# Performance work log

Hardware: AMD Instinct MI355X
Metric: run time of the kernel (lower is better)

The kernel has to match this reference:

```python
import jax, jax.numpy as jnp
import numpy as np

# SS2D (VMamba) dims
B, H, W, C = 2, 48, 48, 96
D_INNER, D_STATE, DT_RANK, K = 192, 32, 6, 4


def _silu(x):
    return x * jax.nn.sigmoid(x)


def setup_inputs() -> dict:
    key = jax.random.key(0)
    ks = jax.random.split(key, 8)
    inputs = jax.random.normal(ks[0], (B, H, W, C), jnp.float32)
    in_proj_w = jax.random.normal(ks[1], (2 * D_INNER, C), jnp.float32) * 0.02
    conv_w = jax.random.normal(ks[2], (D_INNER, 1, 3, 3), jnp.float32) * 0.1
    conv_b = jnp.zeros((D_INNER,), jnp.float32)
    x_proj_w = jax.random.normal(ks[3], (K, DT_RANK + 2 * D_STATE, D_INNER), jnp.float32) * 0.02
    dt_projs_w = jax.random.normal(ks[4], (K, D_INNER, DT_RANK), jnp.float32) * 0.1
    dt_projs_b = jax.random.uniform(ks[5], (K, D_INNER), jnp.float32, -4.0, -2.0)
    # S4D-real init: A_log[n] = log(n+1), tiled over K*d_inner
    A_logs = jnp.log(jnp.tile(jnp.arange(1, D_STATE + 1, dtype=jnp.float32), (K * D_INNER, 1)))
    Ds = jnp.ones((K * D_INNER,), jnp.float32)
    ln_w = jnp.ones((D_INNER,), jnp.float32)
    ln_b = jnp.zeros((D_INNER,), jnp.float32)
    out_proj_w = jax.random.normal(ks[6], (C, D_INNER), jnp.float32) * 0.02
    return dict(inputs=inputs, in_proj_w=in_proj_w, conv_w=conv_w, conv_b=conv_b,
                x_proj_w=x_proj_w, dt_projs_w=dt_projs_w, dt_projs_b=dt_projs_b,
                A_logs=A_logs, Ds=Ds, ln_w=ln_w, ln_b=ln_b, out_proj_w=out_proj_w)


def _selective_scan(us, deltas, A, Bs, Cs, Ds_kd):
    # us, deltas: (B,K,d,L); Bs, Cs: (B,K,N,L); A: (K,d,N); Ds_kd: (K,d)
    u_l = jnp.moveaxis(us, -1, 0)      # (L,B,K,d)
    d_l = jnp.moveaxis(deltas, -1, 0)  # (L,B,K,d)
    B_l = jnp.moveaxis(Bs, -1, 0)      # (L,B,K,N)
    C_l = jnp.moveaxis(Cs, -1, 0)      # (L,B,K,N)
    h0 = jnp.zeros(us.shape[:3] + (A.shape[-1],), us.dtype)  # (B,K,d,N)

    def step(h, inp):
        u, d, b, c = inp
        dA = jnp.exp(d[..., None] * A)                    # (B,K,d,N)
        h = h * dA + (d * u)[..., None] * b[:, :, None, :]
        y = jnp.einsum('bkdn,bkn->bkd', h, c)
        return h, y

    _, ys = jax.lax.scan(step, h0, (u_l, d_l, B_l, C_l))
    ys = jnp.moveaxis(ys, 0, -1)  # (B,K,d,L)
    return ys + Ds_kd[None, :, :, None] * us


def _ss2d(x, in_proj_w, conv_w, conv_b, x_proj_w, dt_projs_w, dt_projs_b,
          A_logs, Ds, ln_w, ln_b, out_proj_w):
    b, h, w, c = x.shape
    L = h * w
    xz = jnp.einsum('bhwc,ec->bhwe', x, in_proj_w)          # (B,H,W,2*d_inner)
    x_, z = jnp.split(xz, 2, axis=-1)
    # depthwise 3x3 conv (NCHW), SAME padding
    x_ = jnp.transpose(x_, (0, 3, 1, 2))                    # (B,d,H,W)
    x_ = jax.lax.conv_general_dilated(x_, conv_w, (1, 1), 'SAME',
                                      feature_group_count=D_INNER,
                                      dimension_numbers=('NCHW', 'OIHW', 'NCHW'))
    x_ = _silu(x_ + conv_b[None, :, None, None])
    # 4-direction scan inputs
    x_hw = x_.reshape(b, D_INNER, L)
    x_wh = jnp.transpose(x_, (0, 1, 3, 2)).reshape(b, D_INNER, L)
    xs = jnp.stack([x_hw, x_wh], axis=1)                    # (B,2,d,L)
    xs = jnp.concatenate([xs, jnp.flip(xs, axis=-1)], axis=1)  # (B,4,d,L)
    x_dbl = jnp.einsum('bkdl,kcd->bkcl', xs, x_proj_w)      # (B,4,dt_rank+2N,L)
    dts = x_dbl[:, :, :DT_RANK]
    Bs = x_dbl[:, :, DT_RANK:DT_RANK + D_STATE]
    Cs = x_dbl[:, :, DT_RANK + D_STATE:]
    dts = jnp.einsum('bkrl,kdr->bkdl', dts, dt_projs_w)
    deltas = jax.nn.softplus(dts + dt_projs_b[None, :, :, None])
    A = -jnp.exp(A_logs).reshape(K, D_INNER, D_STATE)
    Ds_kd = Ds.reshape(K, D_INNER)
    out_y = _selective_scan(xs, deltas, A, Bs, Cs, Ds_kd)   # (B,4,d,L)
    inv_y = jnp.flip(out_y[:, 2:4], axis=-1)                # (B,2,d,L)
    wh_y = jnp.transpose(out_y[:, 1].reshape(b, D_INNER, w, h), (0, 1, 3, 2)).reshape(b, D_INNER, L)
    invwh_y = jnp.transpose(inv_y[:, 1].reshape(b, D_INNER, w, h), (0, 1, 3, 2)).reshape(b, D_INNER, L)
    y = out_y[:, 0] + inv_y[:, 0] + wh_y + invwh_y          # (B,d,L)
    y = jnp.transpose(y, (0, 2, 1)).reshape(b, h, w, D_INNER)
    # LayerNorm over channel dim
    mu = jnp.mean(y, axis=-1, keepdims=True)
    var = jnp.var(y, axis=-1, keepdims=True)
    y = (y - mu) * jax.lax.rsqrt(var + 1e-5) * ln_w + ln_b
    y = y * _silu(z)
    return jnp.einsum('bhwd,cd->bhwc', y, out_proj_w)


def reference(inputs, in_proj_w, conv_w, conv_b, x_proj_w, dt_projs_w, dt_projs_b,
              A_logs, Ds, ln_w, ln_b, out_proj_w):
    attn = _ss2d(inputs, in_proj_w, conv_w, conv_b, x_proj_w, dt_projs_w,
                 dt_projs_b, A_logs, Ds, ln_w, ln_b, out_proj_w)
    return inputs + attn
```

## Files before the change

### kernel.cpp

```cpp
#include <hip/hip_runtime.h>
#include <math.h>

#define B_ 2
#define H_ 48
#define W_ 48
#define C_ 96
#define D_ 192
#define L_ 2304
#define K_ 4
#define NS 32
#define RK 6
#define CD 70

#define NC 16
#define CL (L_/NC)
#define NCH (B_*K_*D_)

#define BDL (B_*D_*L_)
#define OFF_Z      0
#define OFF_XPRE   (OFF_Z    + BDL)
#define OFF_XHW    (OFF_XPRE + BDL)
#define OFF_XWH    (OFF_XHW  + BDL)
#define OFF_DELTA  (OFF_XWH  + BDL)
#define OFF_BS     (OFF_DELTA+ B_*K_*D_*L_)
#define OFF_CS     (OFF_BS   + B_*K_*L_*NS)
#define OFF_YS     (OFF_CS   + B_*K_*L_*NS)
#define OFF_YF     (OFF_YS   + B_*K_*L_*D_)

#define OFF_DU     OFF_YS

#define OFF_H0     OFF_YF

__device__ __forceinline__ float fexp2(float x) {
    float r; asm("v_exp_f32 %0, %1" : "=v"(r) : "v"(x)); return r;
}

__global__ __launch_bounds__(256) void k1_inproj(const float* __restrict__ x,
        const float* __restrict__ w, float* __restrict__ ws) {
    __shared__ __align__(16) float Xs[24*128];
    int blk = blockIdx.x;
    int b = blk / 288;
    int rem = blk % 288;
    int l0 = (rem >> 2) * 32;
    int es = rem & 3;
    int tid = threadIdx.x;
    const float4* xs4 = (const float4*)(x + (size_t)(b*L_ + l0)*C_);
    #pragma unroll
    for (int it = 0; it < 3; ++it) {
        int i4 = it*256 + tid;
        float4 v = xs4[i4];
        int idx4 = i4*4;
        int p = idx4 / 96, c = idx4 % 96;
        *(float4*)&Xs[(c>>2)*128 + p*4] = v;
    }
    __syncthreads();
    int l = tid & 31, eg = tid >> 5;
    int pos = l0 + l;
    float acc[12];
    #pragma unroll
    for (int i = 0; i < 12; ++i) acc[i] = 0.f;
    const float4* wp[12];
    #pragma unroll
    for (int i = 0; i < 12; ++i) {
        int e = es*96 + eg*12 + i;
        wp[i] = (const float4*)(w + (size_t)e*96);
    }
    for (int q = 0; q < 24; ++q) {
        float4 xr = *(const float4*)&Xs[q*128 + l*4];
        #pragma unroll
        for (int i = 0; i < 12; ++i) {
            float4 wv = wp[i][q];
            acc[i] += xr.x*wv.x + xr.y*wv.y + xr.z*wv.z + xr.w*wv.w;
        }
    }
    if (es < 2) {
        float* xpre = ws + OFF_XPRE;
        #pragma unroll
        for (int i = 0; i < 12; ++i) {
            int e = es*96 + eg*12 + i;
            xpre[(size_t)(b*D_ + e)*L_ + pos] = acc[i];
        }
    } else {
        float* zp = ws + OFF_Z + (size_t)(b*L_ + pos)*D_ + (es-2)*96 + eg*12;
        #pragma unroll
        for (int q = 0; q < 3; ++q)
            *(float4*)&zp[q*4] = make_float4(acc[q*4], acc[q*4+1], acc[q*4+2], acc[q*4+3]);
    }
}

__global__ __launch_bounds__(256) void k2_conv(const float* __restrict__ cw,
        const float* __restrict__ cb, float* __restrict__ ws) {
    __shared__ float img[26*48];
    __shared__ float res[24*49];
    int blk = blockIdx.x;
    int bd = blk >> 1;
    int half = blk & 1;
    int d = bd % D_;
    int hh0 = half * 24;
    int tid = threadIdx.x;
    const float* xp = ws + OFF_XPRE + (size_t)bd*L_;
    for (int it = 0; it < 5; ++it) {
        int idx = it*256 + tid;
        if (idx < 26*48) {
            int gr = hh0 - 1 + idx/48;
            img[idx] = (gr >= 0 && gr < H_) ? xp[gr*48 + idx%48] : 0.f;
        }
    }
    float wr[9];
    #pragma unroll
    for (int j = 0; j < 9; ++j) wr[j] = cw[d*9 + j];
    float bias = cb[d];
    __syncthreads();
    float* hw = ws + OFF_XHW + (size_t)bd*L_ + hh0*48;
    for (int it = 0; it < 5; ++it) {
        int idx = it*256 + tid;
        if (idx < 24*48) {
            int r = idx/48, w0 = idx%48;
            float acc = bias;
            #pragma unroll
            for (int kh = 0; kh < 3; ++kh) {
                #pragma unroll
                for (int kw = 0; kw < 3; ++kw) {
                    int iw = w0 + kw - 1;
                    if (iw >= 0 && iw < W_)
                        acc = fmaf(img[(r+kh)*48 + iw], wr[kh*3 + kw], acc);
                }
            }
            float v = acc / (1.f + __expf(-acc));
            hw[idx] = v;
            res[r*49 + w0] = v;
        }
    }
    __syncthreads();
    float* wh = ws + OFF_XWH + (size_t)bd*L_;
    for (int it = 0; it < 5; ++it) {
        int idx = it*256 + tid;
        if (idx < 24*48) {
            int w0 = idx/24, r = idx%24;
            wh[w0*48 + hh0 + r] = res[r*49 + w0];
        }
    }
}

__global__ __launch_bounds__(256) void k3_xproj(const float* __restrict__ xpw,
        const float* __restrict__ dtw, const float* __restrict__ dtb,
        float* __restrict__ ws) {
    __shared__ __align__(16) float Xs[48*64];
    __shared__ float xd[CD*17];
    int blk = blockIdx.x;
    int b = blk / 576;
    int rem = blk % 576;
    int k = rem / 144;
    int l0 = (rem % 144) * 16;
    int tid = threadIdx.x;
    const float* src = ws + ((k & 1) ? OFF_XWH : OFF_XHW);
    bool flip = (k >= 2);
    #pragma unroll
    for (int it = 0; it < 12; ++it) {
        int idx = it*256 + tid;
        int d = idx >> 4, l = idx & 15;
        int pos = flip ? (L_ - 1 - (l0 + l)) : (l0 + l);
        Xs[(d>>2)*64 + l*4 + (d&3)] = src[(size_t)(b*D_ + d)*L_ + pos];
    }
    __syncthreads();
    int l = tid & 15, cg = tid >> 4;
    {
        float acc[5] = {0.f, 0.f, 0.f, 0.f, 0.f};
        const float4* wp[5];
        #pragma unroll
        for (int i = 0; i < 5; ++i) {
            int c = cg + 16*i;
            if (c >= CD) c = 0;
            wp[i] = (const float4*)(xpw + ((size_t)k*CD + c)*D_);
        }
        for (int q = 0; q < 48; ++q) {
            float4 xr = *(const float4*)&Xs[q*64 + l*4];
            #pragma unroll
            for (int i = 0; i < 5; ++i) {
                float4 wv = wp[i][q];
                acc[i] += xr.x*wv.x + xr.y*wv.y + xr.z*wv.z + xr.w*wv.w;
            }
        }
        #pragma unroll
        for (int i = 0; i < 5; ++i) {
            int c = cg + 16*i;
            if (c < CD) xd[c*17 + l] = acc[i];
        }
    }
    __syncthreads();
    {
        float r[6];
        #pragma unroll
        for (int rr = 0; rr < 6; ++rr) r[rr] = xd[rr*17 + l];
        int bk = b*K_ + k;
        float* dout = ws + OFF_DELTA + (size_t)bk*D_*L_;
        int cch = l0 / CL;
        int lc  = l0 - cch*CL + l;
        float* dup = ws + OFF_DU + ((size_t)(bk*NC + cch))*D_*CL;
        int dg = tid >> 4;
        for (int i = 0; i < 12; ++i) {
            int d = dg*12 + i;
            const float* wdt = dtw + ((size_t)k*D_ + d)*6;
            float acc = dtb[k*D_ + d];
            #pragma unroll
            for (int rr = 0; rr < 6; ++rr) acc = fmaf(r[rr], wdt[rr], acc);
            float sp = fmaxf(acc, 0.f) + log1pf(__expf(-fabsf(acc)));
            dout[(size_t)d*L_ + l0 + l] = sp;
            float uv = Xs[(d>>2)*64 + l*4 + (d&3)];
            dup[(size_t)d*CL + lc] = sp * uv;
        }
    }
    {
        float* Bsp = ws + OFF_BS + ((size_t)(b*K_ + k)*L_ + l0)*NS;
        float* Csp = ws + OFF_CS + ((size_t)(b*K_ + k)*L_ + l0)*NS;
        int n = tid & 31, lq = tid >> 5;
        #pragma unroll
        for (int j = 0; j < 2; ++j) {
            int ll = lq + 8*j;
            Bsp[(size_t)ll*NS + n] = xd[(RK + n)*17 + ll];
            Csp[(size_t)ll*NS + n] = xd[(RK + NS + n)*17 + ll];
        }
    }
}

__global__ __launch_bounds__(512) void k4a_local(const float* __restrict__ Alogs,
        float* __restrict__ ws) {
    __shared__ float Pl[2][NC][NS];
    __shared__ float Hl[2][NC][NS];
    int blk = blockIdx.x;
    int bk = blk / 96;
    int p = blk % 96;
    int k = bk & 3;
    int c = threadIdx.x >> 5;
    int n = threadIdx.x & 31;
    int dA = 2*p;
    float aA2 = -__expf(Alogs[((size_t)k*D_ + dA)*NS + n]) * 1.44269504f;
    float aB2 = -__expf(Alogs[((size_t)k*D_ + dA + 1)*NS + n]) * 1.44269504f;
    const float* dpA = ws + OFF_DELTA + (size_t)(bk*D_ + dA)*L_ + c*CL;
    const float* dpB = dpA + L_;
    const float* duA = ws + OFF_DU + ((size_t)(bk*NC + c)*D_ + dA)*CL;
    const float* duB = duA + CL;
    const float* Bsp = ws + OFF_BS + ((size_t)bk*L_ + c*CL)*NS;
    float hA = 0.f, hB = 0.f, PA = 1.f, PB = 1.f;
    #pragma unroll 4
    for (int l = 0; l < CL; ++l) {
        float dlA = dpA[l], dlB = dpB[l];
        float duAv = duA[l], duBv = duB[l];
        float bn = Bsp[l*NS + n];
        float eA = fexp2(dlA * aA2);
        float eB = fexp2(dlB * aB2);
        hA = fmaf(hA, eA, duAv*bn);
        hB = fmaf(hB, eB, duBv*bn);
        PA *= eA;
        PB *= eB;
    }
    Pl[0][c][n] = PA; Pl[1][c][n] = PB;
    Hl[0][c][n] = hA; Hl[1][c][n] = hB;
    __syncthreads();
    if (threadIdx.x < 64) {
        int ch = threadIdx.x >> 5, nn = threadIdx.x & 31;
        float* H0p = ws + OFF_H0 + (size_t)(bk*D_ + dA + ch)*NC*NS + nn;
        float h = 0.f;
        #pragma unroll
        for (int cc = 0; cc < NC; ++cc) {
            H0p[cc*NS] = h;
            h = fmaf(h, Pl[ch][cc][nn], Hl[ch][cc][nn]);
        }
    }
}

__global__ __launch_bounds__(512) void k4c_scan(const float* __restrict__ Alogs,
        float* __restrict__ ws) {
    __shared__ float yld[CL*32];
    int blk = blockIdx.x;
    int dg = blk % 6;
    int c  = (blk / 6) % NC;
    int bk = blk / (6*NC);
    int k = bk & 3;
    int sw = threadIdx.x >> 5;
    int n  = threadIdx.x & 31;
    int dA = dg*32 + sw;
    int dB = dA + 16;
    float aA2 = -__expf(Alogs[((size_t)k*D_ + dA)*NS + n]) * 1.44269504f;
    float aB2 = -__expf(Alogs[((size_t)k*D_ + dB)*NS + n]) * 1.44269504f;
    const float* dpA = ws + OFF_DELTA + (size_t)(bk*D_ + dA)*L_ + c*CL;
    const float* dpB = dpA + 16*L_;
    const float* duA = ws + OFF_DU + ((size_t)(bk*NC + c)*D_ + dA)*CL;
    const float* duB = duA + 16*CL;
    const float* Bsp = ws + OFF_BS + ((size_t)bk*L_ + c*CL)*NS;
    const float* Csp = ws + OFF_CS + ((size_t)bk*L_ + c*CL)*NS;
    float hA = ws[OFF_H0 + (size_t)(bk*D_ + dA)*NC*NS + c*NS + n];
    float hB = ws[OFF_H0 + (size_t)(bk*D_ + dB)*NC*NS + c*NS + n];
    int g = n >> 3;
    int off = ((g & 1) << 1) | (g >> 1);
    for (int lb = 0; lb < CL; lb += 4) {
        float yA[4], yB[4];
        #pragma unroll
        for (int j = 0; j < 4; ++j) {
            int l = lb + j;
            float dlA = dpA[l], dlB = dpB[l];
            float duAv = duA[l], duBv = duB[l];
            float bn = Bsp[l*NS + n];
            float cn = Csp[l*NS + n];
            hA = fmaf(hA, fexp2(dlA*aA2), duAv*bn);
            hB = fmaf(hB, fexp2(dlB*aB2), duBv*bn);
            yA[j] = hA * cn; yB[j] = hB * cn;
        }
        #pragma unroll
        for (int j = 0; j < 4; ++j) {
            yA[j] += __shfl_xor(yA[j], 16);
            yB[j] += __shfl_xor(yB[j], 16);
        }
        float zA0 = (n & 16) ? yA[1] : yA[0];
        float zA1 = (n & 16) ? yA[3] : yA[2];
        float zB0 = (n & 16) ? yB[1] : yB[0];
        float zB1 = (n & 16) ? yB[3] : yB[2];
        zA0 += __shfl_xor(zA0, 8); zA1 += __shfl_xor(zA1, 8);
        zB0 += __shfl_xor(zB0, 8); zB1 += __shfl_xor(zB1, 8);
        float wA = (n & 8) ? zA1 : zA0;
        float wB = (n & 8) ? zB1 : zB0;
        wA += __shfl_xor(wA, 4); wA += __shfl_xor(wA, 2); wA += __shfl_xor(wA, 1);
        wB += __shfl_xor(wB, 4); wB += __shfl_xor(wB, 2); wB += __shfl_xor(wB, 1);
        if ((n & 7) == 0) {
            yld[(lb + off)*32 + sw]      = wA;
            yld[(lb + off)*32 + sw + 16] = wB;
        }
    }
    __syncthreads();
    float* ysp = ws + OFF_YS + (size_t)blk*(CL*32);
    #pragma unroll
    for (int it = 0; it < 9; ++it) {
        int idx = it*512 + threadIdx.x;
        ysp[idx] = yld[idx];
    }
}

__global__ __launch_bounds__(256) void k56_fused(const float* __restrict__ lnw,
        const float* __restrict__ lnb, const float* __restrict__ dsp,
        const float* __restrict__ w, const float* __restrict__ xin,
        float* __restrict__ out, const float* __restrict__ ws) {
    __shared__ __align__(16) float Ys[48*64];
    __shared__ float redS[16][17];
    __shared__ float redQ[16][17];
    __shared__ float muS[16], rsS[16];
    __shared__ float Dsum[D_];
    __shared__ float outT[16*97];
    int blk = blockIdx.x;
    int b = blk / 144;
    int l0 = (blk % 144) * 16;
    int tid = threadIdx.x;
    int hh = l0 / W_;
    int w0b = l0 % W_;
    if (tid < D_) Dsum[tid] = dsp[tid] + dsp[D_+tid] + dsp[2*D_+tid] + dsp[3*D_+tid];
    const float* ysb = ws + OFF_YS;
    int bk0 = b*K_;
    #pragma unroll
    for (int it = 0; it < 3; ++it) {
        int i4 = it*256 + tid;
        int p = i4 / 48, c48 = i4 % 48;
        int pos    = l0 + p;
        int posr   = L_ - 1 - pos;
        int poswh  = (w0b + p)*H_ + hh;
        int poswhr = L_ - 1 - poswh;
        int dsub = c48 >> 3;
        int doff = (c48 & 7) * 4;
        float4 a  = *(const float4*)&ysb[((((size_t)(bk0+0)*NC + pos   /CL)*6 + dsub)*CL + pos   %CL)*32 + doff];
        float4 bb = *(const float4*)&ysb[((((size_t)(bk0+2)*NC + posr  /CL)*6 + dsub)*CL + posr  %CL)*32 + doff];
        float4 cc = *(const float4*)&ysb[((((size_t)(bk0+1)*NC + poswh /CL)*6 + dsub)*CL + poswh %CL)*32 + doff];
        float4 dd = *(const float4*)&ysb[((((size_t)(bk0+3)*NC + poswhr/CL)*6 + dsub)*CL + poswhr%CL)*32 + doff];
        float4 v = make_float4(a.x+bb.x+cc.x+dd.x, a.y+bb.y+cc.y+dd.y,
                               a.z+bb.z+cc.z+dd.z, a.w+bb.w+cc.w+dd.w);
        *(float4*)&Ys[c48*64 + p*4] = v;
    }
    __syncthreads();
    const float* xhw = ws + OFF_XHW;
    #pragma unroll
    for (int it = 0; it < 12; ++it) {
        int idx = it*256 + tid;
        int d = idx >> 4, p = idx & 15;
        float xv = xhw[(size_t)(b*D_ + d)*L_ + l0 + p];
        Ys[(d>>2)*64 + p*4 + (d&3)] += Dsum[d]*xv;
    }
    __syncthreads();
    {
        int p = tid & 15, g = tid >> 4;
        float s = 0.f, q = 0.f;
        #pragma unroll
        for (int j = 0; j < 3; ++j) {
            int qq = g*3 + j;
            #pragma unroll
            for (int sx = 0; sx < 4; ++sx) {
                float v = Ys[qq*64 + p*4 + sx];
                s += v; q += v*v;
            }
        }
        redS[p][g] = s; redQ[p][g] = q;
    }
    __syncthreads();
    if (tid < 16) {
        float s = 0.f, q = 0.f;
        #pragma unroll
        for (int g = 0; g < 16; ++g) { s += redS[tid][g]; q += redQ[tid][g]; }
        float mu  = s * (1.f/192.f);
        float var = q * (1.f/192.f) - mu*mu;
        muS[tid] = mu;
        rsS[tid] = rsqrtf(var + 1e-5f);
    }
    __syncthreads();
    #pragma unroll
    for (int it = 0; it < 3; ++it) {
        int i4 = it*256 + tid;
        int p = i4 / 48, c48 = i4 % 48;
        int pos = l0 + p;
        float4 v  = *(float4*)&Ys[c48*64 + p*4];
        float4 wv = *(const float4*)(lnw + c48*4);
        float4 bv = *(const float4*)(lnb + c48*4);
        float4 zv = *(const float4*)(ws + OFF_Z + (size_t)(b*L_ + pos)*D_ + c48*4);
        float mu = muS[p], rs = rsS[p];
        float o0 = ((v.x-mu)*rs*wv.x + bv.x) * (zv.x / (1.f + __expf(-zv.x)));
        float o1 = ((v.y-mu)*rs*wv.y + bv.y) * (zv.y / (1.f + __expf(-zv.y)));
        float o2 = ((v.z-mu)*rs*wv.z + bv.z) * (zv.z / (1.f + __expf(-zv.z)));
        float o3 = ((v.w-mu)*rs*wv.w + bv.w) * (zv.w / (1.f + __expf(-zv.w)));
        *(float4*)&Ys[c48*64 + p*4] = make_float4(o0, o1, o2, o3);
    }
    __syncthreads();
    int l = tid & 15, cg = tid >> 4;
    float acc[6];
    #pragma unroll
    for (int i = 0; i < 6; ++i) acc[i] = 0.f;
    const float4* wp[6];
    #pragma unroll
    for (int i = 0; i < 6; ++i) {
        int c = cg*6 + i;
        wp[i] = (const float4*)(w + (size_t)c*D_);
    }
    for (int q = 0; q < 48; ++q) {
        float4 xr = *(const float4*)&Ys[q*64 + l*4];
        #pragma unroll
        for (int i = 0; i < 6; ++i) {
            float4 wv = wp[i][q];
            acc[i] += xr.x*wv.x + xr.y*wv.y + xr.z*wv.z + xr.w*wv.w;
        }
    }
    #pragma unroll
    for (int i = 0; i < 6; ++i) outT[l*97 + cg*6 + i] = acc[i];
    __syncthreads();
    #pragma unroll
    for (int it = 0; it < 6; ++it) {
        int idx = it*256 + tid;
        int p = idx / 96, cc = idx % 96;
        size_t o = (size_t)(b*L_ + l0 + p)*C_ + cc;
        out[o] = xin[o] + outT[p*97 + cc];
    }
}

extern "C" void kernel_launch(void* const* d_in, const int* in_sizes, int n_in,
                              void* d_out, int out_size, void* d_ws, size_t ws_size,
                              hipStream_t stream) {
    const float* x        = (const float*)d_in[0];
    const float* in_proj  = (const float*)d_in[1];
    const float* conv_w   = (const float*)d_in[2];
    const float* conv_b   = (const float*)d_in[3];
    const float* x_proj_w = (const float*)d_in[4];
    const float* dt_w     = (const float*)d_in[5];
    const float* dt_b     = (const float*)d_in[6];
    const float* A_logs   = (const float*)d_in[7];
    const float* Ds       = (const float*)d_in[8];
    const float* ln_w     = (const float*)d_in[9];
    const float* ln_b     = (const float*)d_in[10];
    const float* out_w    = (const float*)d_in[11];
    float* out = (float*)d_out;
    float* ws  = (float*)d_ws;

    k1_inproj <<<576,  256, 0, stream>>>(x, in_proj, ws);
    k2_conv   <<<768,  256, 0, stream>>>(conv_w, conv_b, ws);
    k3_xproj  <<<1152, 256, 0, stream>>>(x_proj_w, dt_w, dt_b, ws);
    k4a_local <<<768,  512, 0, stream>>>(A_logs, ws);
    k4c_scan  <<<768,  512, 0, stream>>>(A_logs, ws);
    k56_fused <<<288,  256, 0, stream>>>(ln_w, ln_b, Ds, out_w, x, out, ws);
}
```

Measured before the change: 286.7 us.

## Fuse chunked scan passes into one kernel keeping chunk carries in LDS

The two-pass chunked selective scan (local chunk pass, then a rescan kernel) becomes one kernel per (b,k,d-pair). Chunk carry states stay in shared memory instead of going through global memory, and delta*u is computed on the fly from the conv output rather than precomputed and stored by the x-projection kernel. Scan outputs are written in a plain (bk,d,L) layout, which simplifies the gather in the final fused kernel. In exchange, each block now runs the delta/B/C reads twice and holds a per-block LDS buffer of L float2 values. The fused scan also has only two channels of parallelism per block instead of the previous 32-channel grouping, which could reduce the available occupancy.

```diff
diff --git a/kernel.cpp b/kernel.cpp
--- a/kernel.cpp
+++ b/kernel.cpp
@@ -14,7 +14,6 @@
 
 #define NC 16
 #define CL (L_/NC)
-#define NCH (B_*K_*D_)
 
 #define BDL (B_*D_*L_)
 #define OFF_Z      0
@@ -25,11 +24,6 @@
 #define OFF_BS     (OFF_DELTA+ B_*K_*D_*L_)
 #define OFF_CS     (OFF_BS   + B_*K_*L_*NS)
 #define OFF_YS     (OFF_CS   + B_*K_*L_*NS)
-#define OFF_YF     (OFF_YS   + B_*K_*L_*D_)
-
-#define OFF_DU     OFF_YS
-
-#define OFF_H0     OFF_YF
 
 __device__ __forceinline__ float fexp2(float x) {
     float r; asm("v_exp_f32 %0, %1" : "=v"(r) : "v"(x)); return r;
@@ -194,9 +188,6 @@
         for (int rr = 0; rr < 6; ++rr) r[rr] = xd[rr*17 + l];
         int bk = b*K_ + k;
         float* dout = ws + OFF_DELTA + (size_t)bk*D_*L_;
-        int cch = l0 / CL;
-        int lc  = l0 - cch*CL + l;
-        float* dup = ws + OFF_DU + ((size_t)(bk*NC + cch))*D_*CL;
         int dg = tid >> 4;
         for (int i = 0; i < 12; ++i) {
             int d = dg*12 + i;
@@ -206,8 +197,6 @@
             for (int rr = 0; rr < 6; ++rr) acc = fmaf(r[rr], wdt[rr], acc);
             float sp = fmaxf(acc, 0.f) + log1pf(__expf(-fabsf(acc)));
             dout[(size_t)d*L_ + l0 + l] = sp;
-            float uv = Xs[(d>>2)*64 + l*4 + (d&3)];
-            dup[(size_t)d*CL + lc] = sp * uv;
         }
     }
     {
@@ -223,14 +212,16 @@
     }
 }
 
-__global__ __launch_bounds__(512) void k4a_local(const float* __restrict__ Alogs,
+__global__ __launch_bounds__(512) void k4_fused(const float* __restrict__ Alogs,
         float* __restrict__ ws) {
     __shared__ float Pl[2][NC][NS];
     __shared__ float Hl[2][NC][NS];
+    __shared__ float H0l[2][NC][NS];
+    __shared__ float2 dy[L_];
     int blk = blockIdx.x;
     int bk = blk / 96;
     int p = blk % 96;
-    int k = bk & 3;
+    int b = bk >> 2, k = bk & 3;
     int c = threadIdx.x >> 5;
     int n = threadIdx.x & 31;
     int dA = 2*p;
@@ -238,100 +229,90 @@
     float aB2 = -__expf(Alogs[((size_t)k*D_ + dA + 1)*NS + n]) * 1.44269504f;
     const float* dpA = ws + OFF_DELTA + (size_t)(bk*D_ + dA)*L_ + c*CL;
     const float* dpB = dpA + L_;
-    const float* duA = ws + OFF_DU + ((size_t)(bk*NC + c)*D_ + dA)*CL;
-    const float* duB = duA + CL;
+    const float* uA = ws + ((k & 1) ? OFF_XWH : OFF_XHW) + (size_t)(b*D_ + dA)*L_;
+    const float* uB = uA + L_;
     const float* Bsp = ws + OFF_BS + ((size_t)bk*L_ + c*CL)*NS;
-    float hA = 0.f, hB = 0.f, PA = 1.f, PB = 1.f;
-    #pragma unroll 4
-    for (int l = 0; l < CL; ++l) {
-        float dlA = dpA[l], dlB = dpB[l];
-        float duAv = duA[l], duBv = duB[l];
-        float bn = Bsp[l*NS + n];
-        float eA = fexp2(dlA * aA2);
-        float eB = fexp2(dlB * aB2);
-        hA = fmaf(hA, eA, duAv*bn);
-        hB = fmaf(hB, eB, duBv*bn);
-        PA *= eA;
-        PB *= eB;
-    }
-    Pl[0][c][n] = PA; Pl[1][c][n] = PB;
-    Hl[0][c][n] = hA; Hl[1][c][n] = hB;
+    const float* Csp = ws + OFF_CS + ((size_t)bk*L_ + c*CL)*NS;
+    bool flip = (k >= 2);
+    {
+        float hA = 0.f, hB = 0.f, PA = 1.f, PB = 1.f;
+        #pragma unroll 4
+        for (int l = 0; l < CL; ++l) {
+            int gl = c*CL + l;
+            int gu = flip ? (L_ - 1 - gl) : gl;
+            float dlA = dpA[l], dlB = dpB[l];
+            float uAv = uA[gu], uBv = uB[gu];
+            float duA = dlA*uAv, duB = dlB*uBv;
+            if (n == 0) dy[gl] = make_float2(duA, duB);
+            float bn = Bsp[l*NS + n];
+            float eA = fexp2(dlA * aA2);
+            float eB = fexp2(dlB * aB2);
+            hA = fmaf(hA, eA, duA*bn);
+            hB = fmaf(hB, eB, duB*bn);
+            PA *= eA;
+            PB *= eB;
+        }
+        Pl[0][c][n] = PA; Pl[1][c][n] = PB;
+        Hl[0][c][n] = hA; Hl[1][c][n] = hB;
+    }
     __syncthreads();
     if (threadIdx.x < 64) {
         int ch = threadIdx.x >> 5, nn = threadIdx.x & 31;
-        float* H0p = ws + OFF_H0 + (size_t)(bk*D_ + dA + ch)*NC*NS + nn;
         float h = 0.f;
         #pragma unroll
         for (int cc = 0; cc < NC; ++cc) {
-            H0p[cc*NS] = h;
+            H0l[ch][cc][nn] = h;
             h = fmaf(h, Pl[ch][cc][nn], Hl[ch][cc][nn]);
         }
     }
-}
-
-__global__ __launch_bounds__(512) void k4c_scan(const float* __restrict__ Alogs,
-        float* __restrict__ ws) {
-    __shared__ float yld[CL*32];
-    int blk = blockIdx.x;
-    int dg = blk % 6;
-    int c  = (blk / 6) % NC;
-    int bk = blk / (6*NC);
-    int k = bk & 3;
-    int sw = threadIdx.x >> 5;
-    int n  = threadIdx.x & 31;
-    int dA = dg*32 + sw;
-    int dB = dA + 16;
-    float aA2 = -__expf(Alogs[((size_t)k*D_ + dA)*NS + n]) * 1.44269504f;
-    float aB2 = -__expf(Alogs[((size_t)k*D_ + dB)*NS + n]) * 1.44269504f;
-    const float* dpA = ws + OFF_DELTA + (size_t)(bk*D_ + dA)*L_ + c*CL;
-    const float* dpB = dpA + 16*L_;
-    const float* duA = ws + OFF_DU + ((size_t)(bk*NC + c)*D_ + dA)*CL;
-    const float* duB = duA + 16*CL;
-    const float* Bsp = ws + OFF_BS + ((size_t)bk*L_ + c*CL)*NS;
-    const float* Csp = ws + OFF_CS + ((size_t)bk*L_ + c*CL)*NS;
-    float hA = ws[OFF_H0 + (size_t)(bk*D_ + dA)*NC*NS + c*NS + n];
-    float hB = ws[OFF_H0 + (size_t)(bk*D_ + dB)*NC*NS + c*NS + n];
-    int g = n >> 3;
-    int off = ((g & 1) << 1) | (g >> 1);
-    for (int lb = 0; lb < CL; lb += 4) {
-        float yA[4], yB[4];
-        #pragma unroll
-        for (int j = 0; j < 4; ++j) {
-            int l = lb + j;
-            float dlA = dpA[l], dlB = dpB[l];
-            float duAv = duA[l], duBv = duB[l];
-            float bn = Bsp[l*NS + n];
-            float cn = Csp[l*NS + n];
-            hA = fmaf(hA, fexp2(dlA*aA2), duAv*bn);
-            hB = fmaf(hB, fexp2(dlB*aB2), duBv*bn);
-            yA[j] = hA * cn; yB[j] = hB * cn;
-        }
-        #pragma unroll
-        for (int j = 0; j < 4; ++j) {
-            yA[j] += __shfl_xor(yA[j], 16);
-            yB[j] += __shfl_xor(yB[j], 16);
-        }
-        float zA0 = (n & 16) ? yA[1] : yA[0];
-        float zA1 = (n & 16) ? yA[3] : yA[2];
-        float zB0 = (n & 16) ? yB[1] : yB[0];
-        float zB1 = (n & 16) ? yB[3] : yB[2];
-        zA0 += __shfl_xor(zA0, 8); zA1 += __shfl_xor(zA1, 8);
-        zB0 += __shfl_xor(zB0, 8); zB1 += __shfl_xor(zB1, 8);
-        float wA = (n & 8) ? zA1 : zA0;
-        float wB = (n & 8) ? zB1 : zB0;
-        wA += __shfl_xor(wA, 4); wA += __shfl_xor(wA, 2); wA += __shfl_xor(wA, 1);
-        wB += __shfl_xor(wB, 4); wB += __shfl_xor(wB, 2); wB += __shfl_xor(wB, 1);
-        if ((n & 7) == 0) {
-            yld[(lb + off)*32 + sw]      = wA;
-            yld[(lb + off)*32 + sw + 16] = wB;
-        }
-    }
-    __syncthreads();
-    float* ysp = ws + OFF_YS + (size_t)blk*(CL*32);
+    __syncthreads();
+    {
+        float hA = H0l[0][c][n];
+        float hB = H0l[1][c][n];
+        int g = n >> 3;
+        int off = ((g & 1) << 1) | (g >> 1);
+        for (int lb = 0; lb < CL; lb += 4) {
+            float yA[4], yB[4];
+            #pragma unroll
+            for (int j = 0; j < 4; ++j) {
+                int l = lb + j;
+                float dlA = dpA[l], dlB = dpB[l];
+                float2 du2 = dy[c*CL + l];
+                float bn = Bsp[l*NS + n];
+                float cn = Csp[l*NS + n];
+                hA = fmaf(hA, fexp2(dlA*aA2), du2.x*bn);
+                hB = fmaf(hB, fexp2(dlB*aB2), du2.y*bn);
+                yA[j] = hA * cn; yB[j] = hB * cn;
+            }
+            #pragma unroll
+            for (int j = 0; j < 4; ++j) {
+                yA[j] += __shfl_xor(yA[j], 16);
+                yB[j] += __shfl_xor(yB[j], 16);
+            }
+            float zA0 = (n & 16) ? yA[1] : yA[0];
+            float zA1 = (n & 16) ? yA[3] : yA[2];
+            float zB0 = (n & 16) ? yB[1] : yB[0];
+            float zB1 = (n & 16) ? yB[3] : yB[2];
+            zA0 += __shfl_xor(zA0, 8); zA1 += __shfl_xor(zA1, 8);
+            zB0 += __shfl_xor(zB0, 8); zB1 += __shfl_xor(zB1, 8);
+            float wA = (n & 8) ? zA1 : zA0;
+            float wB = (n & 8) ? zB1 : zB0;
+            wA += __shfl_xor(wA, 4); wA += __shfl_xor(wA, 2); wA += __shfl_xor(wA, 1);
+            wB += __shfl_xor(wB, 4); wB += __shfl_xor(wB, 2); wB += __shfl_xor(wB, 1);
+            if ((n & 7) == 0) {
+                dy[c*CL + lb + off] = make_float2(wA, wB);
+            }
+        }
+    }
+    __syncthreads();
+    float* ysp = ws + OFF_YS + (size_t)(bk*D_ + dA)*L_;
     #pragma unroll
     for (int it = 0; it < 9; ++it) {
         int idx = it*512 + threadIdx.x;
-        ysp[idx] = yld[idx];
+        int row = idx / L_;
+        int l = idx - row*L_;
+        float2 v = dy[l];
+        ysp[(size_t)row*L_ + l] = row ? v.y : v.x;
     }
 }
 
@@ -352,34 +333,24 @@
     int hh = l0 / W_;
     int w0b = l0 % W_;
     if (tid < D_) Dsum[tid] = dsp[tid] + dsp[D_+tid] + dsp[2*D_+tid] + dsp[3*D_+tid];
+    __syncthreads();
     const float* ysb = ws + OFF_YS;
+    const float* xhw = ws + OFF_XHW;
     int bk0 = b*K_;
     #pragma unroll
-    for (int it = 0; it < 3; ++it) {
-        int i4 = it*256 + tid;
-        int p = i4 / 48, c48 = i4 % 48;
+    for (int it = 0; it < 12; ++it) {
+        int idx = it*256 + tid;
+        int d = idx >> 4, p = idx & 15;
         int pos    = l0 + p;
         int posr   = L_ - 1 - pos;
         int poswh  = (w0b + p)*H_ + hh;
         int poswhr = L_ - 1 - poswh;
-        int dsub = c48 >> 3;
-        int doff = (c48 & 7) * 4;
-        float4 a  = *(const float4*)&ysb[((((size_t)(bk0+0)*NC + pos   /CL)*6 + dsub)*CL + pos   %CL)*32 + doff];
-        float4 bb = *(const float4*)&ysb[((((size_t)(bk0+2)*NC + posr  /CL)*6 + dsub)*CL + posr  %CL)*32 + doff];
-        float4 cc = *(const float4*)&ysb[((((size_t)(bk0+1)*NC + poswh /CL)*6 + dsub)*CL + poswh %CL)*32 + doff];
-        float4 dd = *(const float4*)&ysb[((((size_t)(bk0+3)*NC + poswhr/CL)*6 + dsub)*CL + poswhr%CL)*32 + doff];
-        float4 v = make_float4(a.x+bb.x+cc.x+dd.x, a.y+bb.y+cc.y+dd.y,
-                               a.z+bb.z+cc.z+dd.z, a.w+bb.w+cc.w+dd.w);
-        *(float4*)&Ys[c48*64 + p*4] = v;
-    }
-    __syncthreads();
-    const float* xhw = ws + OFF_XHW;
-    #pragma unroll
-    for (int it = 0; it < 12; ++it) {
-        int idx = it*256 + tid;
-        int d = idx >> 4, p = idx & 15;
-        float xv = xhw[(size_t)(b*D_ + d)*L_ + l0 + p];
-        Ys[(d>>2)*64 + p*4 + (d&3)] += Dsum[d]*xv;
+        float y = ysb[((size_t)(bk0+0)*D_ + d)*L_ + pos]
+                + ysb[((size_t)(bk0+2)*D_ + d)*L_ + posr]
+                + ysb[((size_t)(bk0+1)*D_ + d)*L_ + poswh]
+                + ysb[((size_t)(bk0+3)*D_ + d)*L_ + poswhr];
+        float xv = xhw[(size_t)(b*D_ + d)*L_ + pos];
+        Ys[(d>>2)*64 + p*4 + (d&3)] = fmaf(Dsum[d], xv, y);
     }
     __syncthreads();
     {
@@ -475,7 +446,6 @@
     k1_inproj <<<576,  256, 0, stream>>>(x, in_proj, ws);
     k2_conv   <<<768,  256, 0, stream>>>(conv_w, conv_b, ws);
     k3_xproj  <<<1152, 256, 0, stream>>>(x_proj_w, dt_w, dt_b, ws);
-    k4a_local <<<768,  512, 0, stream>>>(A_logs, ws);
-    k4c_scan  <<<768,  512, 0, stream>>>(A_logs, ws);
+    k4_fused  <<<768,  512, 0, stream>>>(A_logs, ws);
     k56_fused <<<288,  256, 0, stream>>>(ln_w, ln_b, Ds, out_w, x, out, ws);
 }
```

Measured after the change: 313.7 us. +9.4%, slower.
